# Performance work log

Hardware: AMD Instinct MI355X
Metric: run time of the kernel (lower is better)

The kernel has to match this reference:

```python
import jax, jax.numpy as jnp
import numpy as np

INPUTDIM = 1024
OUTDIM = 1024
GRIDSIZE = 8


def setup_inputs() -> dict:
    key = jax.random.key(0)
    kx, kc = jax.random.split(key)
    x = jax.random.normal(kx, (8192, INPUTDIM), dtype=jnp.float32)
    scale = 1.0 / (np.sqrt(INPUTDIM) * np.sqrt(GRIDSIZE))
    fouriercoeffs = jax.random.normal(kc, (2, OUTDIM, INPUTDIM, GRIDSIZE), dtype=jnp.float32) * scale
    return {"x": x, "fouriercoeffs": fouriercoeffs}


def reference(x, fouriercoeffs):
    outdim, gridsize = fouriercoeffs.shape[1], fouriercoeffs.shape[3]
    outshape = x.shape[:-1] + (outdim,)
    xf = x.reshape(-1, x.shape[-1])                     # [B, I]
    k = jnp.arange(1, gridsize + 1, dtype=x.dtype)      # [G]
    theta = xf[:, :, None] * k[None, None, :]           # [B, I, G]
    c = jnp.cos(theta)
    s = jnp.sin(theta)
    # y[b,j] = sum_ik c[b,i,k]*W[0,j,i,k] + s[b,i,k]*W[1,j,i,k]
    y = jnp.einsum('bik,jik->bj', c, fouriercoeffs[0]) + \
        jnp.einsum('bik,jik->bj', s, fouriercoeffs[1])
    return y.reshape(outshape)
```

## Files before the change

kernel.cpp:

```cpp
#include <hip/hip_runtime.h>


typedef __attribute__((ext_vector_type(8))) short short8;
typedef __attribute__((ext_vector_type(4))) float f32x4;
typedef __attribute__((ext_vector_type(4))) unsigned int u32x4;

static __device__ __forceinline__ unsigned short f2bf(float f) {
  unsigned u = __builtin_bit_cast(unsigned, f);
  u += 0x7fffu + ((u >> 16) & 1u);
  return (unsigned short)(u >> 16);
}
static __device__ __forceinline__ unsigned int packbf2(float lo, float hi) {
  return (unsigned)f2bf(lo) | ((unsigned)f2bf(hi) << 16);
}

__global__ __launch_bounds__(256) void fkan_pre_a(const float* __restrict__ X,
                                                  float* __restrict__ A2) {
  const unsigned t = blockIdx.x * 256 + threadIdx.x;
  const unsigned il = t & 3, row = (t >> 2) & 8191, kt = t >> 15;
  const float x = X[row * 1024 + kt * 4 + il];
  float s, c;
  __sincosf(x, &s, &c);
  *(float2*)(A2 + (size_t)t * 2) = make_float2(c, s);
}

__global__ __launch_bounds__(256) void fkan_pre_b(const float* __restrict__ W,
                                                  unsigned short* __restrict__ Bq) {
  const unsigned t = blockIdx.x * 256 + threadIdx.x;
  const unsigned i = t & 1023, j = t >> 10;
  const float* w0 = W + (size_t)j * 8192 + i * 8;
  const float* w1 = w0 + 8388608;
  const float4 a0 = *(const float4*)w0, a1 = *(const float4*)(w0 + 4);
  const float4 b0 = *(const float4*)w1, b1 = *(const float4*)(w1 + 4);
  u32x4* out = (u32x4*)(Bq + (size_t)t * 16);
  out[0] = u32x4{packbf2(a0.x, b0.x), packbf2(a0.y, b0.y),
                 packbf2(a0.z, b0.z), packbf2(a0.w, b0.w)};
  out[1] = u32x4{packbf2(a1.x, b1.x), packbf2(a1.y, b1.y),
                 packbf2(a1.z, b1.z), packbf2(a1.w, b1.w)};
}

__global__ __launch_bounds__(256, 2) void fkan_main(
    const float* __restrict__ A2,
    const unsigned short* __restrict__ Bq,
    float* __restrict__ Y) {
  constexpr int KT = 256;
  __shared__ alignas(16) unsigned short Asb[2][128 * 64];
  __shared__ alignas(16) unsigned short Bsb[2][128 * 64];

  const int tid = threadIdx.x;
  const int bn = blockIdx.x & 7, bm = blockIdx.x >> 3;
  const int lane = tid & 63;
  const int w = tid >> 6;
  const int wm = w >> 1, wn = w & 1;

  const int il = tid & 3;
  const int row0 = tid >> 2, row1 = row0 + 64;
  const int e0 = (il * 16) ^ ((row0 & 7) << 3);
  const float* a2p0 = A2 + ((size_t)(bm * 128 + row0) * 4 + il) * 2;
  const float* a2p1 = A2 + ((size_t)(bm * 128 + row1) * 4 + il) * 2;

  const int l3 = lane >> 3, l7 = lane & 7;
  const unsigned short* bsrc[4];
#pragma unroll
  for (int j = 0; j < 4; ++j) {
    const int col_l = w * 32 + j * 8 + l3;
    bsrc[j] = Bq + (size_t)(bn * 128 + col_l) * 16384 + (l7 ^ l3) * 8;
  }

  auto issueB = [&](int kt, int buf) {
#pragma unroll
    for (int j = 0; j < 4; ++j) {
      const unsigned short* src = bsrc[j] + kt * 64;
      unsigned short* dst = &Bsb[buf][(w * 32 + j * 8) * 64];
      __builtin_amdgcn_global_load_lds(
          (const __attribute__((address_space(1))) unsigned int*)src,
          (__attribute__((address_space(3))) unsigned int*)dst, 16, 0, 0);
    }
  };
  auto chebpack = [&](float2 cs, unsigned* pk) {
    const float c1 = cs.x, s1 = cs.y, tc = 2.f * c1;
    float cp = c1, sp = s1;
    float cq = tc * c1 - 1.f, sq = tc * s1;
    pk[0] = packbf2(c1, s1);
    pk[1] = packbf2(cq, sq);
#pragma unroll
    for (int g = 2; g < 8; ++g) {
      const float cn = tc * cq - cp, sn = tc * sq - sp;
      pk[g] = packbf2(cn, sn);
      cp = cq; sp = sq; cq = cn; sq = sn;
    }
  };
  auto writeA = [&](int buf, const unsigned* k0, const unsigned* k1) {
    *(u32x4*)(&Asb[buf][row0 * 64 + e0]) = u32x4{k0[0], k0[1], k0[2], k0[3]};
    *(u32x4*)(&Asb[buf][row0 * 64 + (e0 ^ 8)]) = u32x4{k0[4], k0[5], k0[6], k0[7]};
    *(u32x4*)(&Asb[buf][row1 * 64 + e0]) = u32x4{k1[0], k1[1], k1[2], k1[3]};
    *(u32x4*)(&Asb[buf][row1 * 64 + (e0 ^ 8)]) = u32x4{k1[4], k1[5], k1[6], k1[7]};
  };

  f32x4 acc[4][4];
#pragma unroll
  for (int m = 0; m < 4; ++m)
#pragma unroll
    for (int n = 0; n < 4; ++n) acc[m][n] = f32x4{0.f, 0.f, 0.f, 0.f};

  unsigned k0[8], k1[8];
  {
    chebpack(*(const float2*)a2p0, k0);
    chebpack(*(const float2*)a2p1, k1);
    writeA(0, k0, k1);
    issueB(0, 0);
  }
  float2 avA0 = *(const float2*)(a2p0 + 65536);
  float2 avA1 = *(const float2*)(a2p1 + 65536);
  __syncthreads();

  int buf = 0;
  for (int kt = 0; kt < KT; ++kt) {
    const int nb = buf ^ 1;
    if (kt + 1 < KT) issueB(kt + 1, nb);
    float2 avB0 = avA0, avB1 = avA1;
    if (kt + 2 < KT) {
      avB0 = *(const float2*)(a2p0 + (size_t)(kt + 2) * 65536);
      avB1 = *(const float2*)(a2p1 + (size_t)(kt + 2) * 65536);
    }

    {
      const int sr = (lane & 7) << 3;
      short8 af[2][4], bf_[2][4];
#pragma unroll
      for (int ks = 0; ks < 2; ++ks) {
        const int koff = (ks * 32 + (lane >> 4) * 8) ^ sr;
#pragma unroll
        for (int m = 0; m < 4; ++m)
          af[ks][m] = *(const short8*)(&Asb[buf][(wm * 64 + m * 16 + (lane & 15)) * 64 + koff]);
#pragma unroll
        for (int n = 0; n < 4; ++n)
          bf_[ks][n] = *(const short8*)(&Bsb[buf][(wn * 64 + n * 16 + (lane & 15)) * 64 + koff]);
      }
#pragma unroll
      for (int ks = 0; ks < 2; ++ks)
#pragma unroll
        for (int m = 0; m < 4; ++m)
#pragma unroll
          for (int n = 0; n < 4; ++n)
            acc[m][n] = __builtin_amdgcn_mfma_f32_16x16x32_bf16(
                af[ks][m], bf_[ks][n], acc[m][n], 0, 0, 0);
    }

    if (kt + 1 < KT) {
      chebpack(avA0, k0);
      chebpack(avA1, k1);
      writeA(nb, k0, k1);
    }
    __syncthreads();
    avA0 = avB0; avA1 = avB1;
    buf = nb;
  }

#pragma unroll
  for (int m = 0; m < 4; ++m) {
    const int r0 = bm * 128 + wm * 64 + m * 16 + (lane >> 4) * 4;
#pragma unroll
    for (int n = 0; n < 4; ++n) {
      const int col = bn * 128 + wn * 64 + n * 16 + (lane & 15);
#pragma unroll
      for (int r = 0; r < 4; ++r)
        Y[(size_t)(r0 + r) * 1024 + col] = acc[m][n][r];
    }
  }
}

static __device__ __forceinline__ short8 trig_pack(float xv, int half) {
  float s1, c1;
  __sincosf(xv, &s1, &c1);
  float ca, sa;
  if (half == 0) {
    ca = c1; sa = s1;
  } else {
    const float c2 = c1 * c1 - s1 * s1, s2 = 2.f * s1 * c1;
    const float c4 = c2 * c2 - s2 * s2, s4 = 2.f * s2 * c2;
    ca = c4 * c1 - s4 * s1; sa = s4 * c1 + c4 * s1;
  }
  const float cb = ca * c1 - sa * s1, sb = sa * c1 + ca * s1;
  const float cc = cb * c1 - sb * s1, sc = sb * c1 + cb * s1;
  const float cd = cc * c1 - sc * s1, sd = sc * c1 + cc * s1;
  short8 v;
  v[0] = (short)f2bf(ca); v[1] = (short)f2bf(sa);
  v[2] = (short)f2bf(cb); v[3] = (short)f2bf(sb);
  v[4] = (short)f2bf(cc); v[5] = (short)f2bf(sc);
  v[6] = (short)f2bf(cd); v[7] = (short)f2bf(sd);
  return v;
}
static __device__ __forceinline__ short8 pack_w(float4 w0, float4 w1) {
  short8 v;
  v[0] = (short)f2bf(w0.x); v[1] = (short)f2bf(w1.x);
  v[2] = (short)f2bf(w0.y); v[3] = (short)f2bf(w1.y);
  v[4] = (short)f2bf(w0.z); v[5] = (short)f2bf(w1.z);
  v[6] = (short)f2bf(w0.w); v[7] = (short)f2bf(w1.w);
  return v;
}

__global__ __launch_bounds__(256, 2) void fkan_fallback(
    const float* __restrict__ X, const float* __restrict__ W,
    float* __restrict__ Y) {
  constexpr int N = 1024, KT = 256;
  __shared__ alignas(16) unsigned short Asb[128 * 64];
  __shared__ alignas(16) unsigned short Bsb[128 * 64];
  const int tid = threadIdx.x;
  const int bm = blockIdx.x & 63;
  const int bn = blockIdx.x >> 6;
  const int lane = tid & 63;
  const int w = tid >> 6;
  const int wm = w >> 1, wn = w & 1;
  const float* W0 = W;
  const float* W1 = W + 8388608;
  const int rowbase = tid >> 3;
  const int il = (tid & 7) >> 1;
  const int half = tid & 1;
  const int sst = (rowbase & 7) << 3;
  const int aoff0 = rowbase * 64 + ((il * 16 + half * 8) ^ sst);
  const size_t xaddr0 = (size_t)(bm * 128 + rowbase) * 1024 + il;
  const size_t wbase0 = (size_t)(bn * 128 + rowbase) * 8192 + il * 8 + half * 4;

  f32x4 acc[4][4];
#pragma unroll
  for (int m = 0; m < 4; ++m)
#pragma unroll
    for (int n = 0; n < 4; ++n) acc[m][n] = f32x4{0.f, 0.f, 0.f, 0.f};

  float xq[4];
  float4 wq0[4], wq1[4];
#pragma unroll
  for (int p = 0; p < 4; ++p) {
    xq[p] = X[xaddr0 + p * 32768];
    wq0[p] = *(const float4*)(W0 + wbase0 + p * 262144);
    wq1[p] = *(const float4*)(W1 + wbase0 + p * 262144);
  }

  for (int kt = 0; kt < KT; ++kt) {
    short8 va[4], vb[4];
#pragma unroll
    for (int p = 0; p < 4; ++p) {
      va[p] = trig_pack(xq[p], half);
      vb[p] = pack_w(wq0[p], wq1[p]);
    }
    __syncthreads();
#pragma unroll
    for (int p = 0; p < 4; ++p) {
      *(short8*)(Asb + aoff0 + p * 2048) = va[p];
      *(short8*)(Bsb + aoff0 + p * 2048) = vb[p];
    }
    const int ktn = (kt < KT - 1) ? kt + 1 : kt;
    const size_t xo = xaddr0 + (size_t)ktn * 4;
    const size_t wo = wbase0 + (size_t)ktn * 32;
#pragma unroll
    for (int p = 0; p < 4; ++p) {
      xq[p] = X[xo + p * 32768];
      wq0[p] = *(const float4*)(W0 + wo + p * 262144);
      wq1[p] = *(const float4*)(W1 + wo + p * 262144);
    }
    __syncthreads();
    const int sr = (lane & 7) << 3;
    short8 af[2][4], bf_[2][4];
#pragma unroll
    for (int ks = 0; ks < 2; ++ks) {
      const int koff = ks * 32 + (lane >> 4) * 8;
#pragma unroll
      for (int m = 0; m < 4; ++m)
        af[ks][m] = *(const short8*)(Asb + (wm * 64 + m * 16 + (lane & 15)) * 64 + (koff ^ sr));
#pragma unroll
      for (int n = 0; n < 4; ++n)
        bf_[ks][n] = *(const short8*)(Bsb + (wn * 64 + n * 16 + (lane & 15)) * 64 + (koff ^ sr));
    }
#pragma unroll
    for (int ks = 0; ks < 2; ++ks)
#pragma unroll
      for (int m = 0; m < 4; ++m)
#pragma unroll
        for (int n = 0; n < 4; ++n)
          acc[m][n] = __builtin_amdgcn_mfma_f32_16x16x32_bf16(
              af[ks][m], bf_[ks][n], acc[m][n], 0, 0, 0);
  }
#pragma unroll
  for (int m = 0; m < 4; ++m) {
    const int r0 = bm * 128 + wm * 64 + m * 16 + (lane >> 4) * 4;
#pragma unroll
    for (int n = 0; n < 4; ++n) {
      const int col = bn * 128 + wn * 64 + n * 16 + (lane & 15);
#pragma unroll
      for (int r = 0; r < 4; ++r)
        Y[(size_t)(r0 + r) * N + col] = acc[m][n][r];
    }
  }
}

extern "C" void kernel_launch(void* const* d_in, const int* in_sizes, int n_in,
                              void* d_out, int out_size, void* d_ws, size_t ws_size,
                              hipStream_t stream) {
  const float* x = (const float*)d_in[0];
  const float* w = (const float*)d_in[1];
  float* y = (float*)d_out;
  constexpr size_t A2_BYTES = 67108864ull;
  constexpr size_t BQ_BYTES = 33554432ull;
  if (ws_size >= A2_BYTES + BQ_BYTES) {
    float* a2 = (float*)d_ws;
    unsigned short* bq = (unsigned short*)((char*)d_ws + A2_BYTES);
    fkan_pre_a<<<dim3(32768), dim3(256), 0, stream>>>(x, a2);
    fkan_pre_b<<<dim3(4096), dim3(256), 0, stream>>>(w, bq);
    fkan_main<<<dim3(512), dim3(256), 0, stream>>>(a2, bq, y);
  } else {
    fkan_fallback<<<dim3(512), dim3(256), 0, stream>>>(x, w, y);
  }
}
```

Measured before the change: 469.8 us.

## Widen main GEMM tile to 128x256 with 512 threads and row-major trig buffer

```diff
diff --git a/kernel.cpp b/kernel.cpp
--- a/kernel.cpp
+++ b/kernel.cpp
@@ -1,34 +1,41 @@
 #include <hip/hip_runtime.h>
+#include <hip/hip_bf16.h>
 
 
 typedef __attribute__((ext_vector_type(8))) short short8;
 typedef __attribute__((ext_vector_type(4))) float f32x4;
 typedef __attribute__((ext_vector_type(4))) unsigned int u32x4;
 
-static __device__ __forceinline__ unsigned short f2bf(float f) {
+static __device__ __forceinline__ unsigned short f2bf_rne(float f) {
   unsigned u = __builtin_bit_cast(unsigned, f);
   u += 0x7fffu + ((u >> 16) & 1u);
   return (unsigned short)(u >> 16);
 }
 static __device__ __forceinline__ unsigned int packbf2(float lo, float hi) {
-  return (unsigned)f2bf(lo) | ((unsigned)f2bf(hi) << 16);
+  const unsigned short a = __builtin_bit_cast(unsigned short, __float2bfloat16(lo));
+  const unsigned short b = __builtin_bit_cast(unsigned short, __float2bfloat16(hi));
+  return (unsigned)a | ((unsigned)b << 16);
 }
 
 __global__ __launch_bounds__(256) void fkan_pre_a(const float* __restrict__ X,
                                                   float* __restrict__ A2) {
-  const unsigned t = blockIdx.x * 256 + threadIdx.x;
-  const unsigned il = t & 3, row = (t >> 2) & 8191, kt = t >> 15;
-  const float x = X[row * 1024 + kt * 4 + il];
-  float s, c;
-  __sincosf(x, &s, &c);
-  *(float2*)(A2 + (size_t)t * 2) = make_float2(c, s);
+  const int row = blockIdx.x;
+  const int k = threadIdx.x;
+  const float4 xv = *(const float4*)(X + (size_t)row * 1024 + k * 4);
+  float s0, c0, s1, c1, s2, c2, s3, c3;
+  __sincosf(xv.x, &s0, &c0);
+  __sincosf(xv.y, &s1, &c1);
+  __sincosf(xv.z, &s2, &c2);
+  __sincosf(xv.w, &s3, &c3);
+  float* out = A2 + (size_t)row * 2048 + k * 8;
+  *(f32x4*)out = f32x4{c0, s0, c1, s1};
+  *(f32x4*)(out + 4) = f32x4{c2, s2, c3, s3};
 }
 
 __global__ __launch_bounds__(256) void fkan_pre_b(const float* __restrict__ W,
                                                   unsigned short* __restrict__ Bq) {
   const unsigned t = blockIdx.x * 256 + threadIdx.x;
-  const unsigned i = t & 1023, j = t >> 10;
-  const float* w0 = W + (size_t)j * 8192 + i * 8;
+  const float* w0 = W + (size_t)t * 8;
   const float* w1 = w0 + 8388608;
   const float4 a0 = *(const float4*)w0, a1 = *(const float4*)(w0 + 4);
   const float4 b0 = *(const float4*)w1, b1 = *(const float4*)(w1 + 4);
@@ -39,32 +46,31 @@
                  packbf2(a1.z, b1.z), packbf2(a1.w, b1.w)};
 }
 
-__global__ __launch_bounds__(256, 2) void fkan_main(
+__global__ __launch_bounds__(512, 2) void fkan_main(
     const float* __restrict__ A2,
     const unsigned short* __restrict__ Bq,
     float* __restrict__ Y) {
   constexpr int KT = 256;
   __shared__ alignas(16) unsigned short Asb[2][128 * 64];
-  __shared__ alignas(16) unsigned short Bsb[2][128 * 64];
+  __shared__ alignas(16) unsigned short Bsb[2][256 * 64];
 
   const int tid = threadIdx.x;
-  const int bn = blockIdx.x & 7, bm = blockIdx.x >> 3;
+  const int bnp = blockIdx.x & 3, bm = blockIdx.x >> 2;
   const int lane = tid & 63;
   const int w = tid >> 6;
-  const int wm = w >> 1, wn = w & 1;
+  const int wm = w >> 2, wn = w & 3;
 
   const int il = tid & 3;
-  const int row0 = tid >> 2, row1 = row0 + 64;
+  const int row0 = tid >> 2;
   const int e0 = (il * 16) ^ ((row0 & 7) << 3);
-  const float* a2p0 = A2 + ((size_t)(bm * 128 + row0) * 4 + il) * 2;
-  const float* a2p1 = A2 + ((size_t)(bm * 128 + row1) * 4 + il) * 2;
+  const float* a2p0 = A2 + (size_t)(bm * 128 + row0) * 2048 + il * 2;
 
   const int l3 = lane >> 3, l7 = lane & 7;
   const unsigned short* bsrc[4];
 #pragma unroll
   for (int j = 0; j < 4; ++j) {
     const int col_l = w * 32 + j * 8 + l3;
-    bsrc[j] = Bq + (size_t)(bn * 128 + col_l) * 16384 + (l7 ^ l3) * 8;
+    bsrc[j] = Bq + (size_t)(bnp * 256 + col_l) * 16384 + (l7 ^ l3) * 8;
   }
 
   auto issueB = [&](int kt, int buf) {
@@ -90,11 +96,9 @@
       cp = cq; sp = sq; cq = cn; sq = sn;
     }
   };
-  auto writeA = [&](int buf, const unsigned* k0, const unsigned* k1) {
+  auto writeA = [&](int buf, const unsigned* k0) {
     *(u32x4*)(&Asb[buf][row0 * 64 + e0]) = u32x4{k0[0], k0[1], k0[2], k0[3]};
     *(u32x4*)(&Asb[buf][row0 * 64 + (e0 ^ 8)]) = u32x4{k0[4], k0[5], k0[6], k0[7]};
-    *(u32x4*)(&Asb[buf][row1 * 64 + e0]) = u32x4{k1[0], k1[1], k1[2], k1[3]};
-    *(u32x4*)(&Asb[buf][row1 * 64 + (e0 ^ 8)]) = u32x4{k1[4], k1[5], k1[6], k1[7]};
   };
 
   f32x4 acc[4][4];
@@ -103,26 +107,21 @@
 #pragma unroll
     for (int n = 0; n < 4; ++n) acc[m][n] = f32x4{0.f, 0.f, 0.f, 0.f};
 
-  unsigned k0[8], k1[8];
+  unsigned k0[8];
   {
     chebpack(*(const float2*)a2p0, k0);
-    chebpack(*(const float2*)a2p1, k1);
-    writeA(0, k0, k1);
+    writeA(0, k0);
     issueB(0, 0);
   }
-  float2 avA0 = *(const float2*)(a2p0 + 65536);
-  float2 avA1 = *(const float2*)(a2p1 + 65536);
+  float2 avA = *(const float2*)(a2p0 + 8);
   __syncthreads();
 
   int buf = 0;
   for (int kt = 0; kt < KT; ++kt) {
     const int nb = buf ^ 1;
     if (kt + 1 < KT) issueB(kt + 1, nb);
-    float2 avB0 = avA0, avB1 = avA1;
-    if (kt + 2 < KT) {
-      avB0 = *(const float2*)(a2p0 + (size_t)(kt + 2) * 65536);
-      avB1 = *(const float2*)(a2p1 + (size_t)(kt + 2) * 65536);
-    }
+    float2 avB = avA;
+    if (kt + 2 < KT) avB = *(const float2*)(a2p0 + (size_t)(kt + 2) * 8);
 
     {
       const int sr = (lane & 7) << 3;
@@ -148,12 +147,11 @@
     }
 
     if (kt + 1 < KT) {
-      chebpack(avA0, k0);
-      chebpack(avA1, k1);
-      writeA(nb, k0, k1);
+      chebpack(avA, k0);
+      writeA(nb, k0);
     }
     __syncthreads();
-    avA0 = avB0; avA1 = avB1;
+    avA = avB;
     buf = nb;
   }
 
@@ -162,7 +160,7 @@
     const int r0 = bm * 128 + wm * 64 + m * 16 + (lane >> 4) * 4;
 #pragma unroll
     for (int n = 0; n < 4; ++n) {
-      const int col = bn * 128 + wn * 64 + n * 16 + (lane & 15);
+      const int col = bnp * 256 + wn * 64 + n * 16 + (lane & 15);
 #pragma unroll
       for (int r = 0; r < 4; ++r)
         Y[(size_t)(r0 + r) * 1024 + col] = acc[m][n][r];
@@ -185,18 +183,18 @@
   const float cc = cb * c1 - sb * s1, sc = sb * c1 + cb * s1;
   const float cd = cc * c1 - sc * s1, sd = sc * c1 + cc * s1;
   short8 v;
-  v[0] = (short)f2bf(ca); v[1] = (short)f2bf(sa);
-  v[2] = (short)f2bf(cb); v[3] = (short)f2bf(sb);
-  v[4] = (short)f2bf(cc); v[5] = (short)f2bf(sc);
-  v[6] = (short)f2bf(cd); v[7] = (short)f2bf(sd);
+  v[0] = (short)f2bf_rne(ca); v[1] = (short)f2bf_rne(sa);
+  v[2] = (short)f2bf_rne(cb); v[3] = (short)f2bf_rne(sb);
+  v[4] = (short)f2bf_rne(cc); v[5] = (short)f2bf_rne(sc);
+  v[6] = (short)f2bf_rne(cd); v[7] = (short)f2bf_rne(sd);
   return v;
 }
 static __device__ __forceinline__ short8 pack_w(float4 w0, float4 w1) {
   short8 v;
-  v[0] = (short)f2bf(w0.x); v[1] = (short)f2bf(w1.x);
-  v[2] = (short)f2bf(w0.y); v[3] = (short)f2bf(w1.y);
-  v[4] = (short)f2bf(w0.z); v[5] = (short)f2bf(w1.z);
-  v[6] = (short)f2bf(w0.w); v[7] = (short)f2bf(w1.w);
+  v[0] = (short)f2bf_rne(w0.x); v[1] = (short)f2bf_rne(w1.x);
+  v[2] = (short)f2bf_rne(w0.y); v[3] = (short)f2bf_rne(w1.y);
+  v[4] = (short)f2bf_rne(w0.z); v[5] = (short)f2bf_rne(w1.z);
+  v[6] = (short)f2bf_rne(w0.w); v[7] = (short)f2bf_rne(w1.w);
   return v;
 }
 
@@ -305,9 +303,9 @@
   if (ws_size >= A2_BYTES + BQ_BYTES) {
     float* a2 = (float*)d_ws;
     unsigned short* bq = (unsigned short*)((char*)d_ws + A2_BYTES);
-    fkan_pre_a<<<dim3(32768), dim3(256), 0, stream>>>(x, a2);
+    fkan_pre_a<<<dim3(8192), dim3(256), 0, stream>>>(x, a2);
     fkan_pre_b<<<dim3(4096), dim3(256), 0, stream>>>(w, bq);
-    fkan_main<<<dim3(512), dim3(256), 0, stream>>>(a2, bq, y);
+    fkan_main<<<dim3(256), dim3(512), 0, stream>>>(a2, bq, y);
   } else {
     fkan_fallback<<<dim3(512), dim3(256), 0, stream>>>(x, w, y);
   }
```

Result: no change. 467.5 us (-0.5%).
